# Optimization experiments

Hardware: AMD Instinct MI355X
Metric: run time of the kernel (lower is better)

The kernel has to match this reference:

```python
import jax, jax.numpy as jnp
import numpy as np

# quantization / activation scales (stand-ins for act_scales dict entries)
S_IN = 0.05      # in_proj:input
S_Z = 0.02       # in_proj:output (also gate/z scale)
S_U = 0.01       # x_proj:input (conv output scale)
S_DTLN = 0.02    # dt_layernorm:output
S_B = 0.02       # B_layernorm:output
S_C = 0.02       # C_layernorm:output
S_DT = 0.01      # dt_proj:output
S_Y = 0.01       # out_proj:input
EPS = 1e-6
R = 128          # time_step_rank
N = 16           # ssm_state_size


def qa(x, s):
    # simulate int8 activation quantization (values kept in fp32)
    return jnp.clip(jnp.round(x / s), -128.0, 127.0)


def qw(w):
    # per-tensor symmetric int8 weight quantization
    s = jnp.max(jnp.abs(w)) / 127.0
    return jnp.clip(jnp.round(w / s), -128.0, 127.0), s


def rmsnorm_q(x, w, s):
    x = x.astype(jnp.float32)
    x = x * jax.lax.rsqrt(jnp.mean(x * x, axis=-1, keepdims=True) + EPS)
    return qa(w * x, s)


def ssm_scan(u, dt, A, Bm, Cm):
    # u, dt: [B, D, S]; Bm, Cm: [B, S, N]; A: [D, N]
    def step(h, xs):
        dt_t, u_t, B_t, C_t = xs                     # [B,D],[B,D],[B,N],[B,N]
        dA = jnp.exp(dt_t[..., None] * A)            # [B,D,N]
        h = h * dA + (dt_t * u_t)[..., None] * B_t[:, None, :]
        y = jnp.einsum('bdn,bn->bd', h, C_t)
        return h, y
    Bsz, Dd, S = u.shape
    h0 = jnp.zeros((Bsz, Dd, A.shape[1]), u.dtype)
    xs = (jnp.moveaxis(dt, 2, 0), jnp.moveaxis(u, 2, 0),
          jnp.moveaxis(Bm, 1, 0), jnp.moveaxis(Cm, 1, 0))
    _, ys = jax.lax.scan(step, h0, xs)               # ys: [S,B,D]
    return jnp.moveaxis(ys, 0, 2)                    # [B,D,S]


def setup_inputs() -> dict:
    key = jax.random.key(0)
    ks = jax.random.split(key, 10)
    B, S, H, Din, K = 2, 2048, 2048, 4096, 4
    return {
        'hidden_states': jax.random.normal(ks[0], (B, S, H), jnp.float32),
        'in_proj_w': jax.random.normal(ks[1], (2 * Din, H), jnp.float32) * 0.02,
        'conv_w': jax.random.normal(ks[2], (Din, K), jnp.float32) * 0.1,
        'conv_b': jax.random.normal(ks[3], (Din,), jnp.float32) * 0.01,
        'x_proj_w': jax.random.normal(ks[4], (R + 2 * N, Din), jnp.float32) * 0.02,
        'dt_ln_w': jnp.ones((R,), jnp.float32),
        'B_ln_w': jnp.ones((N,), jnp.float32),
        'C_ln_w': jnp.ones((N,), jnp.float32),
        'dt_proj_w': jax.random.normal(ks[5], (Din, R), jnp.float32) * 0.05,
        'dt_bias': jax.random.normal(ks[6], (Din,), jnp.float32) * 0.5 - 4.0,
        'A_log': jnp.log(jnp.broadcast_to(jnp.arange(1, N + 1, dtype=jnp.float32), (Din, N))),
        'D_skip': jnp.ones((Din,), jnp.float32),
        'out_proj_w': jax.random.normal(ks[7], (H, Din), jnp.float32) * 0.02,
    }


def reference(hidden_states, in_proj_w, conv_w, conv_b, x_proj_w, dt_ln_w,
              B_ln_w, C_ln_w, dt_proj_w, dt_bias, A_log, D_skip, out_proj_w):
    # --- in_proj (W8A8B8O8), then seqlen-last layout [B, 2D, S] ---
    x_q = qa(hidden_states, S_IN)
    wq, ws = qw(in_proj_w)
    proj_q = qa((x_q @ wq.T) * (S_IN * ws), S_Z)          # [B,S,2D] int8-valued
    proj_q = jnp.swapaxes(proj_q, 1, 2)                   # [B,2D,S]
    Din = proj_q.shape[1] // 2
    hs_q, gate_q = proj_q[:, :Din], proj_q[:, Din:]

    # --- quantized causal depthwise conv1d + silu (QCausalConv1D) ---
    cwq, cws = qw(conv_w)
    K = conv_w.shape[1]
    conv_out = jax.lax.conv_general_dilated(
        hs_q, cwq[:, None, :], (1,), [(K - 1, 0)],
        dimension_numbers=('NCH', 'OIH', 'NCH'), feature_group_count=Din)
    conv_out = conv_out * (S_Z * cws) + conv_b[None, :, None]
    u_q = qa(jax.nn.silu(conv_out), S_U)                  # [B,Din,S]

    # --- x_proj (W8A8BF16OF16) -> dt/B/C, inner RMSNorms + quant ---
    xwq, xws = qw(x_proj_w)
    ssm_p = (jnp.swapaxes(u_q, 1, 2) @ xwq.T) * (S_U * xws)   # [B,S,R+2N] float
    dt_q = rmsnorm_q(ssm_p[..., :R], dt_ln_w, S_DTLN)
    B_q = rmsnorm_q(ssm_p[..., R:R + N], B_ln_w, S_B)
    C_q = rmsnorm_q(ssm_p[..., R + N:], C_ln_w, S_C)

    # --- dt_proj (W8A8B8O8, bias folded into scan) ---
    dwq, dws = qw(dt_proj_w)
    dt8 = qa((dt_q @ dwq.T) * (S_DTLN * dws), S_DT)       # [B,S,Din]
    dt = jax.nn.softplus(jnp.swapaxes(dt8, 1, 2) * S_DT + dt_bias[None, :, None])

    # --- selective scan (QSScan): dequantize, recur, gate ---
    u = u_q * S_U
    A = -jnp.exp(A_log)
    ys = ssm_scan(u, dt, A, B_q * S_B, C_q * S_C)         # [B,Din,S]
    ys = ys + u * D_skip[None, :, None]
    ys = ys * jax.nn.silu(gate_q * S_Z)

    # --- QAct + out_proj (W8A8BF16OF16) ---
    y_q = qa(jnp.swapaxes(ys, 1, 2), S_Y)                 # [B,S,Din]
    owq, ows = qw(out_proj_w)
    return (y_q @ owq.T) * (S_Y * ows)                    # [B,S,H]
```

## Files before the change

### kernel.cpp

```cpp
#include <hip/hip_runtime.h>
#include <stdint.h>

typedef signed char i8;
typedef int v4i __attribute__((ext_vector_type(4)));

#define S_IN  0.05f
#define S_Z   0.02f
#define S_U   0.01f
#define S_DTLN 0.02f
#define S_B   0.02f
#define S_C   0.02f
#define S_DT  0.01f
#define S_Y   0.01f

__device__ __forceinline__ int dot4(int a, int b, int c) {
    return __builtin_amdgcn_sdot4(a, b, c, false);
}

__device__ __forceinline__ float q8f(float x, float s) {
    float r = rintf(x / s);
    return fmaxf(-128.0f, fminf(127.0f, r));
}
__device__ __forceinline__ int q8i(float x, float s) { return (int)q8f(x, s); }

__device__ __forceinline__ float softplus_f(float x) {
    return __fadd_rn(fmaxf(x, 0.0f), log1pf(expf(-fabsf(x))));
}

__device__ __forceinline__ int sbyte_of(int w, int j) {
    return (int)(signed char)((unsigned)w >> (j * 8));
}

__device__ __forceinline__ void gload16(const i8* g, i8* lds) {
    __builtin_amdgcn_global_load_lds(
        (const __attribute__((address_space(1))) unsigned int*)g,
        (__attribute__((address_space(3))) unsigned int*)lds,
        16, 0, 0);
}

__global__ __launch_bounds__(256)
void k_maxabs(const float* __restrict__ w, long long n, unsigned* __restrict__ out) {
    unsigned m = 0;
    long long stride = (long long)gridDim.x * 256;
    for (long long i = (long long)blockIdx.x * 256 + threadIdx.x; i < n; i += stride)
        m = max(m, __float_as_uint(fabsf(w[i])));
    #pragma unroll
    for (int off = 32; off; off >>= 1) {
        unsigned o = (unsigned)__shfl_xor((int)m, off);
        m = max(m, o);
    }
    __shared__ unsigned sm[4];
    if ((threadIdx.x & 63) == 0) sm[threadIdx.x >> 6] = m;
    __syncthreads();
    if (threadIdx.x == 0) {
        unsigned r = max(max(sm[0], sm[1]), max(sm[2], sm[3]));
        atomicMax(out, r);
    }
}

__global__ __launch_bounds__(256)
void k_quant_w(const float* __restrict__ w, long long n,
               const unsigned* __restrict__ maxbits, i8* __restrict__ o) {
    long long i = ((long long)blockIdx.x * 256 + threadIdx.x) * 4;
    if (i >= n) return;
    float s = __uint_as_float(*maxbits) / 127.0f;
    float4 v = *(const float4*)(w + i);
    unsigned pk = ((unsigned)(q8i(v.x, s) & 255))
                | ((unsigned)(q8i(v.y, s) & 255) << 8)
                | ((unsigned)(q8i(v.z, s) & 255) << 16)
                | ((unsigned)(q8i(v.w, s) & 255) << 24);
    *(unsigned*)(o + i) = pk;
}

__global__ __launch_bounds__(256)
void k_quant_x(const float* __restrict__ x, long long n, float s, i8* __restrict__ o) {
    long long i = ((long long)blockIdx.x * 256 + threadIdx.x) * 4;
    if (i >= n) return;
    float4 v = *(const float4*)(x + i);
    unsigned pk = ((unsigned)(q8i(v.x, s) & 255))
                | ((unsigned)(q8i(v.y, s) & 255) << 8)
                | ((unsigned)(q8i(v.z, s) & 255) << 16)
                | ((unsigned)(q8i(v.w, s) & 255) << 24);
    *(unsigned*)(o + i) = pk;
}

template<int EPI>
__global__ __launch_bounds__(256)
void k_gemm(const i8* __restrict__ A, const i8* __restrict__ Bw,
            int M, int N, int K,
            const unsigned* __restrict__ wmaxbits,
            void* __restrict__ out0, void* __restrict__ out1) {
    __shared__ int As[64][17];
    __shared__ int Bs[64][17];
    const int tid = threadIdx.x;
    const int m0 = blockIdx.y << 6;
    const int n0 = blockIdx.x << 6;
    const int tx = tid & 15;
    const int ty = tid >> 4;
    const int ldr = tid >> 2;
    const int ldw = (tid & 3) << 2;
    int acc[4][4] = {};
    for (int k0 = 0; k0 < K; k0 += 64) {
        int4 av = *(const int4*)(A + (size_t)(m0 + ldr) * K + k0 + (ldw << 2));
        int4 bv = make_int4(0, 0, 0, 0);
        if (n0 + ldr < N)
            bv = *(const int4*)(Bw + (size_t)(n0 + ldr) * K + k0 + (ldw << 2));
        As[ldr][ldw + 0] = av.x; As[ldr][ldw + 1] = av.y;
        As[ldr][ldw + 2] = av.z; As[ldr][ldw + 3] = av.w;
        Bs[ldr][ldw + 0] = bv.x; Bs[ldr][ldw + 1] = bv.y;
        Bs[ldr][ldw + 2] = bv.z; Bs[ldr][ldw + 3] = bv.w;
        __syncthreads();
        #pragma unroll
        for (int kk = 0; kk < 16; kk++) {
            const int a0 = As[(ty << 2) + 0][kk];
            const int a1 = As[(ty << 2) + 1][kk];
            const int a2 = As[(ty << 2) + 2][kk];
            const int a3 = As[(ty << 2) + 3][kk];
            const int b0 = Bs[(tx << 2) + 0][kk];
            const int b1 = Bs[(tx << 2) + 1][kk];
            const int b2 = Bs[(tx << 2) + 2][kk];
            const int b3 = Bs[(tx << 2) + 3][kk];
            acc[0][0] = dot4(a0, b0, acc[0][0]); acc[0][1] = dot4(a0, b1, acc[0][1]);
            acc[0][2] = dot4(a0, b2, acc[0][2]); acc[0][3] = dot4(a0, b3, acc[0][3]);
            acc[1][0] = dot4(a1, b0, acc[1][0]); acc[1][1] = dot4(a1, b1, acc[1][1]);
            acc[1][2] = dot4(a1, b2, acc[1][2]); acc[1][3] = dot4(a1, b3, acc[1][3]);
            acc[2][0] = dot4(a2, b0, acc[2][0]); acc[2][1] = dot4(a2, b1, acc[2][1]);
            acc[2][2] = dot4(a2, b2, acc[2][2]); acc[2][3] = dot4(a2, b3, acc[2][3]);
            acc[3][0] = dot4(a3, b0, acc[3][0]); acc[3][1] = dot4(a3, b1, acc[3][1]);
            acc[3][2] = dot4(a3, b2, acc[3][2]); acc[3][3] = dot4(a3, b3, acc[3][3]);
        }
        __syncthreads();
    }
    const float wsc = __uint_as_float(*wmaxbits) / 127.0f;
    if constexpr (EPI == 1) {
        const float sc = S_U * wsc;
        float* O = (float*)out0;
        const int j0 = n0 + (tx << 2);
        #pragma unroll
        for (int r = 0; r < 4; r++) {
            const int m = m0 + (ty << 2) + r;
            if (j0 + 3 < N) {
                float4 v;
                v.x = (float)acc[r][0] * sc; v.y = (float)acc[r][1] * sc;
                v.z = (float)acc[r][2] * sc; v.w = (float)acc[r][3] * sc;
                *(float4*)(O + (size_t)m * N + j0) = v;
            } else {
                for (int c = 0; c < 4; c++)
                    if (j0 + c < N) O[(size_t)m * N + j0 + c] = (float)acc[r][c] * sc;
            }
        }
    }
}

template<int EPI>
__global__ __launch_bounds__(256)
void k_mgemm(const i8* __restrict__ A, const i8* __restrict__ Bw,
             int M, int N, int K,
             const unsigned* __restrict__ wmaxbits,
             void* __restrict__ out0, void* __restrict__ out1) {
    __shared__ i8 sA[8192];
    __shared__ i8 sB[8192];
    const int tid = threadIdx.x;
    const int w = tid >> 6;
    const int l = tid & 63;
    const int m0 = blockIdx.y << 7;
    const int n0 = blockIdx.x << 7;
    const int lr = l & 15;
    const int lk = l >> 4;
    const i8* gA0 = A  + (size_t)(m0 + (w * 16) + lr) * K + lk * 16;
    const i8* gA1 = A  + (size_t)(m0 + ((4 + w) * 16) + lr) * K + lk * 16;
    const i8* gB0 = Bw + (size_t)(n0 + (w * 16) + lr) * K + lk * 16;
    const i8* gB1 = Bw + (size_t)(n0 + ((4 + w) * 16) + lr) * K + lk * 16;
    i8* lA0 = sA + (w * 1024);
    i8* lA1 = sA + ((4 + w) * 1024);
    i8* lB0 = sB + (w * 1024);
    i8* lB1 = sB + ((4 + w) * 1024);
    const int mw = (w >> 1) * 4;
    const int nw = (w & 1) * 4;
    const int rdoff = lk * 256 + lr * 16;
    v4i acc[4][4] = {};
    for (int k0 = 0; k0 < K; k0 += 64) {
        gload16(gA0 + k0, lA0);
        gload16(gA1 + k0, lA1);
        gload16(gB0 + k0, lB0);
        gload16(gB1 + k0, lB1);
        __syncthreads();
        v4i af[4], bf[4];
        #pragma unroll
        for (int t = 0; t < 4; t++) {
            af[t] = *(const v4i*)(sA + (mw + t) * 1024 + rdoff);
            bf[t] = *(const v4i*)(sB + (nw + t) * 1024 + rdoff);
        }
        #pragma unroll
        for (int mt = 0; mt < 4; mt++)
            #pragma unroll
            for (int nt = 0; nt < 4; nt++)
                acc[mt][nt] = __builtin_amdgcn_mfma_i32_16x16x64_i8(af[mt], bf[nt], acc[mt][nt], 0, 0, 0);
        __syncthreads();
    }
    const float wsc = __uint_as_float(*wmaxbits) / 127.0f;
    const int m0w = m0 + (w >> 1) * 64;
    const int n0w = n0 + (w & 1) * 64;
    if constexpr (EPI == 0 || EPI == 2) {
        const float sc = (EPI == 0 ? S_IN : S_DTLN) * wsc;
        const float qs = (EPI == 0 ? S_Z : S_DT);
        const int b = m0w >> 11;
        #pragma unroll
        for (int nt = 0; nt < 4; nt++) {
            const int j = n0w + nt * 16 + lr;
            i8* dst;
            if constexpr (EPI == 0) dst = (j < 4096) ? (i8*)out0 : (i8*)out1;
            else dst = (i8*)out0;
            const int jj = j & 4095;
            #pragma unroll
            for (int mt = 0; mt < 4; mt++) {
                const int sbase = (m0w & 2047) + mt * 16 + lk * 4;
                unsigned pk = 0;
                #pragma unroll
                for (int r = 0; r < 4; r++) {
                    float v = (float)acc[mt][nt][r] * sc;
                    pk |= ((unsigned)(q8i(v, qs) & 255)) << (8 * r);
                }
                *(unsigned*)(dst + ((size_t)b * 4096 + jj) * 2048 + sbase) = pk;
            }
        }
    } else {
        const float sc = S_Y * wsc;
        float* O = (float*)out0;
        #pragma unroll
        for (int mt = 0; mt < 4; mt++)
            #pragma unroll
            for (int r = 0; r < 4; r++) {
                const int m = m0w + mt * 16 + lk * 4 + r;
                #pragma unroll
                for (int nt = 0; nt < 4; nt++)
                    O[(size_t)m * N + n0w + nt * 16 + lr] = (float)acc[mt][nt][r] * sc;
            }
    }
}

__global__ __launch_bounds__(256)
void k_conv(const i8* __restrict__ hsq, const i8* __restrict__ cwq,
            const float* __restrict__ conv_b, const unsigned* __restrict__ cmaxbits,
            i8* __restrict__ uq, i8* __restrict__ uqT) {
    __shared__ char lt[64][68];
    const int tid = threadIdx.x;
    const int b = blockIdx.z;
    const int d0 = blockIdx.y << 6;
    const int s0 = blockIdx.x << 6;
    const int dl = tid >> 2;
    const int sg = tid & 3;
    const int d = d0 + dl;
    const int sbase = s0 + (sg << 4);
    const i8* xp = hsq + ((size_t)b * 4096 + d) * 2048;
    int v[19];
    #pragma unroll
    for (int i = 0; i < 19; i++) {
        int s = sbase - 3 + i;
        v[i] = (s >= 0) ? (int)xp[s] : 0;
    }
    const unsigned cw = *(const unsigned*)(cwq + (size_t)d * 4);
    const int w0 = (int)(char)(cw & 255);
    const int w1 = (int)(char)((cw >> 8) & 255);
    const int w2 = (int)(char)((cw >> 16) & 255);
    const int w3 = (int)(char)((cw >> 24) & 255);
    const float cws = __uint_as_float(*cmaxbits) / 127.0f;
    const float sc = S_Z * cws;
    const float bias = conv_b[d];
    unsigned pk[4] = {0, 0, 0, 0};
    #pragma unroll
    for (int t = 0; t < 16; t++) {
        int acc = v[t] * w0 + v[t + 1] * w1 + v[t + 2] * w2 + v[t + 3] * w3;
        float f = __fadd_rn(__fmul_rn((float)acc, sc), bias);
        float sig = 1.0f / (1.0f + expf(-f));
        float sl = __fmul_rn(f, sig);
        int q = q8i(sl, S_U);
        pk[t >> 2] |= ((unsigned)(q & 255)) << ((t & 3) * 8);
        lt[(sg << 4) + t][dl] = (char)q;
    }
    *(int4*)(uq + ((size_t)b * 4096 + d) * 2048 + sbase) = make_int4(pk[0], pk[1], pk[2], pk[3]);
    __syncthreads();
    const int rr = tid >> 2;
    const int wg = tid & 3;
    const int* rp = (const int*)(&lt[rr][wg << 4]);
    int4 o; o.x = rp[0]; o.y = rp[1]; o.z = rp[2]; o.w = rp[3];
    *(int4*)(uqT + ((size_t)b * 2048 + s0 + rr) * 4096 + d0 + (wg << 4)) = o;
}

__global__ __launch_bounds__(64)
void k_rms(const float* __restrict__ p,
           const float* __restrict__ wdt, const float* __restrict__ wB, const float* __restrict__ wC,
           i8* __restrict__ dtq, i8* __restrict__ bqT, i8* __restrict__ cqT) {
    const int row = blockIdx.x;
    const int lane = threadIdx.x;
    const float* x = p + (size_t)row * 160;
    float a0 = x[lane], a1 = x[64 + lane];
    float bb = (lane < 16) ? x[128 + lane] : 0.0f;
    float cc = (lane < 16) ? x[144 + lane] : 0.0f;
    float sdt = __fadd_rn(__fmul_rn(a0, a0), __fmul_rn(a1, a1));
    float sB = __fmul_rn(bb, bb);
    float sC = __fmul_rn(cc, cc);
    #pragma unroll
    for (int off = 32; off; off >>= 1) {
        sdt = __fadd_rn(sdt, __shfl_xor(sdt, off));
        sB  = __fadd_rn(sB,  __shfl_xor(sB, off));
        sC  = __fadd_rn(sC,  __shfl_xor(sC, off));
    }
    float rdt = 1.0f / sqrtf(sdt / 128.0f + 1e-6f);
    float rB  = 1.0f / sqrtf(sB / 16.0f + 1e-6f);
    float rC  = 1.0f / sqrtf(sC / 16.0f + 1e-6f);
    dtq[(size_t)row * 128 + lane]      = (i8)q8i(__fmul_rn(wdt[lane],      __fmul_rn(a0, rdt)), S_DTLN);
    dtq[(size_t)row * 128 + 64 + lane] = (i8)q8i(__fmul_rn(wdt[64 + lane], __fmul_rn(a1, rdt)), S_DTLN);
    if (lane < 16) {
        size_t tpos = ((size_t)(row >> 11) * 16 + lane) * 2048 + (row & 2047);
        bqT[tpos] = (i8)q8i(__fmul_rn(wB[lane], __fmul_rn(bb, rB)), S_B);
        cqT[tpos] = (i8)q8i(__fmul_rn(wC[lane], __fmul_rn(cc, rC)), S_C);
    }
}

__global__ __launch_bounds__(256)
void k_lut_dt(const float* __restrict__ dt_bias, float* __restrict__ lut) {
    const int d = blockIdx.x;
    const int q = threadIdx.x;
    const float bias = dt_bias[d];
    lut[(size_t)d * 256 + q] =
        softplus_f(__fadd_rn(__fmul_rn((float)(q - 128), S_DT), bias));
}
__global__ __launch_bounds__(256)
void k_lut_silu(float* __restrict__ lut) {
    const int q = threadIdx.x;
    float gv = __fmul_rn((float)(q - 128), S_Z);
    float sg = __fmul_rn(gv, 1.0f / (1.0f + expf(-gv)));
    lut[q] = sg;
}

__global__ __launch_bounds__(256)
void k_scan3(const i8* __restrict__ dt8, const i8* __restrict__ uq, const i8* __restrict__ gq,
             const i8* __restrict__ BqT, const i8* __restrict__ CqT,
             const float* __restrict__ lut_dt, const float* __restrict__ lut_silu,
             const float* __restrict__ A_log, const float* __restrict__ D_skip,
             i8* __restrict__ yq) {
    const int g = blockIdx.x * 256 + threadIdx.x;
    const int n = g & 15;
    const int bd = g >> 4;
    const int d = bd & 4095;
    const int b = bd >> 12;
    const float Acoef = -expf(A_log[(size_t)d * 16 + n]);
    const float Dd = D_skip[d];
    const float* ldt = lut_dt + (size_t)d * 256;
    const v4i* dtp = (const v4i*)(dt8 + (size_t)bd * 2048);
    const v4i* up  = (const v4i*)(uq  + (size_t)bd * 2048);
    const v4i* gp  = (const v4i*)(gq  + (size_t)bd * 2048);
    const v4i* Bp  = (const v4i*)(BqT + ((size_t)b * 16 + n) * 2048);
    const v4i* Cp  = (const v4i*)(CqT + ((size_t)b * 16 + n) * 2048);
    i8* yp = yq + (size_t)b * 2048 * 4096 + d;
    float h = 0.0f;
    v4i dtw = dtp[0], uw = up[0], gw = gp[0], bw = Bp[0], cw = Cp[0];
    for (int t = 0; t < 128; t++) {
        v4i ndt, nu, ng, nb, nc;
        if (t < 127) { ndt = dtp[t + 1]; nu = up[t + 1]; ng = gp[t + 1]; nb = Bp[t + 1]; nc = Cp[t + 1]; }
        float dtv[16], dA[16];
        #pragma unroll
        for (int j = 0; j < 16; j++)
            dtv[j] = ldt[sbyte_of(dtw[j >> 2], j & 3) + 128];
        #pragma unroll
        for (int j = 0; j < 16; j++)
            dA[j] = expf(__fmul_rn(dtv[j], Acoef));
        float ysave = 0.0f;
        #pragma unroll
        for (int j = 0; j < 16; j++) {
            float uv = __fmul_rn((float)sbyte_of(uw[j >> 2], j & 3), S_U);
            float Bv = __fmul_rn((float)sbyte_of(bw[j >> 2], j & 3), S_B);
            float Cv = __fmul_rn((float)sbyte_of(cw[j >> 2], j & 3), S_C);
            h = __fadd_rn(__fmul_rn(h, dA[j]), __fmul_rn(__fmul_rn(dtv[j], uv), Bv));
            float y = __fmul_rn(h, Cv);
            y = __fadd_rn(y, __shfl_xor(y, 1));
            y = __fadd_rn(y, __shfl_xor(y, 2));
            y = __fadd_rn(y, __shfl_xor(y, 4));
            y = __fadd_rn(y, __shfl_xor(y, 8));
            if (j == n) ysave = y;
        }
        int uws = (n & 8) ? ((n & 4) ? uw[3] : uw[2]) : ((n & 4) ? uw[1] : uw[0]);
        int gws = (n & 8) ? ((n & 4) ? gw[3] : gw[2]) : ((n & 4) ? gw[1] : gw[0]);
        float uvn = __fmul_rn((float)(int)(signed char)((unsigned)uws >> ((n & 3) * 8)), S_U);
        int gb = (int)(signed char)((unsigned)gws >> ((n & 3) * 8));
        float ys = __fadd_rn(ysave, __fmul_rn(uvn, Dd));
        float sg = lut_silu[gb + 128];
        float vv = __fmul_rn(ys, sg);
        yp[(size_t)(t * 16 + n) * 4096] = (i8)q8i(vv, S_Y);
        if (t < 127) { dtw = ndt; uw = nu; gw = ng; bw = nb; cw = nc; }
    }
}

extern "C" void kernel_launch(void* const* d_in, const int* in_sizes, int n_in,
                              void* d_out, int out_size, void* d_ws, size_t ws_size,
                              hipStream_t stream) {
    const float* hidden   = (const float*)d_in[0];
    const float* in_proj  = (const float*)d_in[1];
    const float* conv_w   = (const float*)d_in[2];
    const float* conv_b   = (const float*)d_in[3];
    const float* x_proj   = (const float*)d_in[4];
    const float* dt_ln    = (const float*)d_in[5];
    const float* B_ln     = (const float*)d_in[6];
    const float* C_ln     = (const float*)d_in[7];
    const float* dt_proj  = (const float*)d_in[8];
    const float* dt_bias  = (const float*)d_in[9];
    const float* A_log    = (const float*)d_in[10];
    const float* D_skip   = (const float*)d_in[11];
    const float* out_proj = (const float*)d_in[12];
    float* out = (float*)d_out;

    char* ws = (char*)d_ws;
    unsigned* scales = (unsigned*)ws;
    i8* WQ   = (i8*)(ws + 256);
    i8* XQ   = (i8*)(ws + 16777472);
    i8* HSQ  = (i8*)(ws + 25166080);
    char* S0 = ws + 41943296;
    float* SSMP = (float*)S0;
    i8* DTQb = (i8*)(S0 + 2621440);
    i8* XWQ  = (i8*)(S0 + 3145728);
    i8* DWQ  = (i8*)(S0 + 3801088);
    i8* CWQ  = (i8*)(S0 + 4325376);
    float* LUTDT = (float*)S0;
    float* LUTSI = (float*)(S0 + 4194304);
    i8* BQT  = (i8*)(S0 + 4341760);
    i8* CQT  = (i8*)(S0 + 4407296);

    i8* GQ = (i8*)d_out;
    i8* UQ = (i8*)d_out + 16777216;
    i8* UQT = WQ;
    i8* OWQ = XQ;
    i8* DT8 = HSQ;
    i8* YQ  = WQ;

    hipMemsetAsync(scales, 0, 256, stream);

    k_maxabs<<<2048, 256, 0, stream>>>(in_proj, 16777216LL, scales + 0);
    k_maxabs<<<64,   256, 0, stream>>>(conv_w,  16384LL,    scales + 1);
    k_maxabs<<<512,  256, 0, stream>>>(x_proj,  655360LL,   scales + 2);
    k_maxabs<<<512,  256, 0, stream>>>(dt_proj, 524288LL,   scales + 3);
    k_maxabs<<<1024, 256, 0, stream>>>(out_proj, 8388608LL, scales + 4);

    k_quant_w<<<16384, 256, 0, stream>>>(in_proj, 16777216LL, scales + 0, WQ);
    k_quant_w<<<16,    256, 0, stream>>>(conv_w,  16384LL,    scales + 1, CWQ);
    k_quant_w<<<640,   256, 0, stream>>>(x_proj,  655360LL,   scales + 2, XWQ);
    k_quant_w<<<512,   256, 0, stream>>>(dt_proj, 524288LL,   scales + 3, DWQ);
    k_quant_x<<<8192,  256, 0, stream>>>(hidden,  8388608LL,  S_IN, XQ);

    k_mgemm<0><<<dim3(64, 32), 256, 0, stream>>>(XQ, WQ, 4096, 8192, 2048, scales + 0, HSQ, GQ);

    k_quant_w<<<8192, 256, 0, stream>>>(out_proj, 8388608LL, scales + 4, OWQ);

    dim3 gc(32, 64, 2);
    k_conv<<<gc, 256, 0, stream>>>(HSQ, CWQ, conv_b, scales + 1, UQ, UQT);

    dim3 g2(3, 64);
    k_gemm<1><<<g2, 256, 0, stream>>>(UQT, XWQ, 4096, 160, 4096, scales + 2, SSMP, nullptr);

    k_rms<<<4096, 64, 0, stream>>>(SSMP, dt_ln, B_ln, C_ln, DTQb, BQT, CQT);

    k_mgemm<2><<<dim3(32, 32), 256, 0, stream>>>(DTQb, DWQ, 4096, 4096, 128, scales + 3, DT8, nullptr);

    k_lut_dt<<<4096, 256, 0, stream>>>(dt_bias, LUTDT);
    k_lut_silu<<<1, 256, 0, stream>>>(LUTSI);

    k_scan3<<<512, 256, 0, stream>>>(DT8, UQ, GQ, BQT, CQT, LUTDT, LUTSI, A_log, D_skip, YQ);

    k_mgemm<3><<<dim3(16, 32), 256, 0, stream>>>(YQ, OWQ, 4096, 2048, 4096, scales + 4, out, nullptr);
}
```

Baseline: 787.8 us.

## Route x_proj through matrix-core GEMM and batch scan output reductions

The x_proj GEMM moves from the scalar sdot4 tiled kernel to the MFMA-based k_mgemm path. The weight is zero-padded to 256 rows in a fresh buffer, and a new epilogue writes only the first 160 columns. Separately, the scan kernel's 16 per-step shuffle-reduction chains (4 shuffles each) become a recursive-halving butterfly that exchanges half the partial sums at each level, so each lane ends with its own state's sum using fewer shuffles. The cost is an extra memset, wasted compute on the padded columns, and more register pressure in the scan.

```diff
diff --git a/kernel.cpp b/kernel.cpp
--- a/kernel.cpp
+++ b/kernel.cpp
@@ -12,10 +12,6 @@
 #define S_C   0.02f
 #define S_DT  0.01f
 #define S_Y   0.01f
-
-__device__ __forceinline__ int dot4(int a, int b, int c) {
-    return __builtin_amdgcn_sdot4(a, b, c, false);
-}
 
 __device__ __forceinline__ float q8f(float x, float s) {
     float r = rintf(x / s);
@@ -82,74 +78,6 @@
                 | ((unsigned)(q8i(v.z, s) & 255) << 16)
                 | ((unsigned)(q8i(v.w, s) & 255) << 24);
     *(unsigned*)(o + i) = pk;
-}
-
-template<int EPI>
-__global__ __launch_bounds__(256)
-void k_gemm(const i8* __restrict__ A, const i8* __restrict__ Bw,
-            int M, int N, int K,
-            const unsigned* __restrict__ wmaxbits,
-            void* __restrict__ out0, void* __restrict__ out1) {
-    __shared__ int As[64][17];
-    __shared__ int Bs[64][17];
-    const int tid = threadIdx.x;
-    const int m0 = blockIdx.y << 6;
-    const int n0 = blockIdx.x << 6;
-    const int tx = tid & 15;
-    const int ty = tid >> 4;
-    const int ldr = tid >> 2;
-    const int ldw = (tid & 3) << 2;
-    int acc[4][4] = {};
-    for (int k0 = 0; k0 < K; k0 += 64) {
-        int4 av = *(const int4*)(A + (size_t)(m0 + ldr) * K + k0 + (ldw << 2));
-        int4 bv = make_int4(0, 0, 0, 0);
-        if (n0 + ldr < N)
-            bv = *(const int4*)(Bw + (size_t)(n0 + ldr) * K + k0 + (ldw << 2));
-        As[ldr][ldw + 0] = av.x; As[ldr][ldw + 1] = av.y;
-        As[ldr][ldw + 2] = av.z; As[ldr][ldw + 3] = av.w;
-        Bs[ldr][ldw + 0] = bv.x; Bs[ldr][ldw + 1] = bv.y;
-        Bs[ldr][ldw + 2] = bv.z; Bs[ldr][ldw + 3] = bv.w;
-        __syncthreads();
-        #pragma unroll
-        for (int kk = 0; kk < 16; kk++) {
-            const int a0 = As[(ty << 2) + 0][kk];
-            const int a1 = As[(ty << 2) + 1][kk];
-            const int a2 = As[(ty << 2) + 2][kk];
-            const int a3 = As[(ty << 2) + 3][kk];
-            const int b0 = Bs[(tx << 2) + 0][kk];
-            const int b1 = Bs[(tx << 2) + 1][kk];
-            const int b2 = Bs[(tx << 2) + 2][kk];
-            const int b3 = Bs[(tx << 2) + 3][kk];
-            acc[0][0] = dot4(a0, b0, acc[0][0]); acc[0][1] = dot4(a0, b1, acc[0][1]);
-            acc[0][2] = dot4(a0, b2, acc[0][2]); acc[0][3] = dot4(a0, b3, acc[0][3]);
-            acc[1][0] = dot4(a1, b0, acc[1][0]); acc[1][1] = dot4(a1, b1, acc[1][1]);
-            acc[1][2] = dot4(a1, b2, acc[1][2]); acc[1][3] = dot4(a1, b3, acc[1][3]);
-            acc[2][0] = dot4(a2, b0, acc[2][0]); acc[2][1] = dot4(a2, b1, acc[2][1]);
-            acc[2][2] = dot4(a2, b2, acc[2][2]); acc[2][3] = dot4(a2, b3, acc[2][3]);
-            acc[3][0] = dot4(a3, b0, acc[3][0]); acc[3][1] = dot4(a3, b1, acc[3][1]);
-            acc[3][2] = dot4(a3, b2, acc[3][2]); acc[3][3] = dot4(a3, b3, acc[3][3]);
-        }
-        __syncthreads();
-    }
-    const float wsc = __uint_as_float(*wmaxbits) / 127.0f;
-    if constexpr (EPI == 1) {
-        const float sc = S_U * wsc;
-        float* O = (float*)out0;
-        const int j0 = n0 + (tx << 2);
-        #pragma unroll
-        for (int r = 0; r < 4; r++) {
-            const int m = m0 + (ty << 2) + r;
-            if (j0 + 3 < N) {
-                float4 v;
-                v.x = (float)acc[r][0] * sc; v.y = (float)acc[r][1] * sc;
-                v.z = (float)acc[r][2] * sc; v.w = (float)acc[r][3] * sc;
-                *(float4*)(O + (size_t)m * N + j0) = v;
-            } else {
-                for (int c = 0; c < 4; c++)
-                    if (j0 + c < N) O[(size_t)m * N + j0 + c] = (float)acc[r][c] * sc;
-            }
-        }
-    }
 }
 
 template<int EPI>
@@ -224,6 +152,21 @@
                 *(unsigned*)(dst + ((size_t)b * 4096 + jj) * 2048 + sbase) = pk;
             }
         }
+    } else if constexpr (EPI == 1) {
+        const float sc = S_U * wsc;
+        float* O = (float*)out0;
+        #pragma unroll
+        for (int mt = 0; mt < 4; mt++)
+            #pragma unroll
+            for (int r = 0; r < 4; r++) {
+                const int m = m0w + mt * 16 + lk * 4 + r;
+                #pragma unroll
+                for (int nt = 0; nt < 4; nt++) {
+                    const int j = n0w + nt * 16 + lr;
+                    if (j < 160)
+                        O[(size_t)m * 160 + j] = (float)acc[mt][nt][r] * sc;
+                }
+            }
     } else {
         const float sc = S_Y * wsc;
         float* O = (float*)out0;
@@ -335,7 +278,7 @@
 }
 
 __global__ __launch_bounds__(256)
-void k_scan3(const i8* __restrict__ dt8, const i8* __restrict__ uq, const i8* __restrict__ gq,
+void k_scan4(const i8* __restrict__ dt8, const i8* __restrict__ uq, const i8* __restrict__ gq,
              const i8* __restrict__ BqT, const i8* __restrict__ CqT,
              const float* __restrict__ lut_dt, const float* __restrict__ lut_silu,
              const float* __restrict__ A_log, const float* __restrict__ D_skip,
@@ -359,26 +302,59 @@
     for (int t = 0; t < 128; t++) {
         v4i ndt, nu, ng, nb, nc;
         if (t < 127) { ndt = dtp[t + 1]; nu = up[t + 1]; ng = gp[t + 1]; nb = Bp[t + 1]; nc = Cp[t + 1]; }
-        float dtv[16], dA[16];
+        float dtv[16], dA[16], pj[16], Cv[16], y[16];
         #pragma unroll
         for (int j = 0; j < 16; j++)
             dtv[j] = ldt[sbyte_of(dtw[j >> 2], j & 3) + 128];
         #pragma unroll
         for (int j = 0; j < 16; j++)
             dA[j] = expf(__fmul_rn(dtv[j], Acoef));
-        float ysave = 0.0f;
         #pragma unroll
         for (int j = 0; j < 16; j++) {
             float uv = __fmul_rn((float)sbyte_of(uw[j >> 2], j & 3), S_U);
             float Bv = __fmul_rn((float)sbyte_of(bw[j >> 2], j & 3), S_B);
-            float Cv = __fmul_rn((float)sbyte_of(cw[j >> 2], j & 3), S_C);
-            h = __fadd_rn(__fmul_rn(h, dA[j]), __fmul_rn(__fmul_rn(dtv[j], uv), Bv));
-            float y = __fmul_rn(h, Cv);
-            y = __fadd_rn(y, __shfl_xor(y, 1));
-            y = __fadd_rn(y, __shfl_xor(y, 2));
-            y = __fadd_rn(y, __shfl_xor(y, 4));
-            y = __fadd_rn(y, __shfl_xor(y, 8));
-            if (j == n) ysave = y;
+            Cv[j] = __fmul_rn((float)sbyte_of(cw[j >> 2], j & 3), S_C);
+            pj[j] = __fmul_rn(__fmul_rn(dtv[j], uv), Bv);
+        }
+        #pragma unroll
+        for (int j = 0; j < 16; j++) {
+            h = __fadd_rn(__fmul_rn(h, dA[j]), pj[j]);
+            y[j] = __fmul_rn(h, Cv[j]);
+        }
+        float w8[8];
+        #pragma unroll
+        for (int i = 0; i < 8; i++) {
+            float a = y[2 * i], bq = y[2 * i + 1];
+            float snd = (n & 1) ? a : bq;
+            float rcv = __shfl_xor(snd, 1);
+            float kept = (n & 1) ? bq : a;
+            w8[i] = __fadd_rn(kept, rcv);
+        }
+        float w4[4];
+        #pragma unroll
+        for (int i = 0; i < 4; i++) {
+            float a = w8[2 * i], bq = w8[2 * i + 1];
+            float snd = (n & 2) ? a : bq;
+            float rcv = __shfl_xor(snd, 2);
+            float kept = (n & 2) ? bq : a;
+            w4[i] = __fadd_rn(kept, rcv);
+        }
+        float w2[2];
+        #pragma unroll
+        for (int i = 0; i < 2; i++) {
+            float a = w4[2 * i], bq = w4[2 * i + 1];
+            float snd = (n & 4) ? a : bq;
+            float rcv = __shfl_xor(snd, 4);
+            float kept = (n & 4) ? bq : a;
+            w2[i] = __fadd_rn(kept, rcv);
+        }
+        float ysave;
+        {
+            float a = w2[0], bq = w2[1];
+            float snd = (n & 8) ? a : bq;
+            float rcv = __shfl_xor(snd, 8);
+            float kept = (n & 8) ? bq : a;
+            ysave = __fadd_rn(kept, rcv);
         }
         int uws = (n & 8) ? ((n & 4) ? uw[3] : uw[2]) : ((n & 4) ? uw[1] : uw[0]);
         int gws = (n & 8) ? ((n & 4) ? gw[3] : gw[2]) : ((n & 4) ? gw[1] : gw[0]);
@@ -417,14 +393,14 @@
     i8* HSQ  = (i8*)(ws + 25166080);
     char* S0 = ws + 41943296;
     float* SSMP = (float*)S0;
-    i8* DTQb = (i8*)(S0 + 2621440);
-    i8* XWQ  = (i8*)(S0 + 3145728);
-    i8* DWQ  = (i8*)(S0 + 3801088);
-    i8* CWQ  = (i8*)(S0 + 4325376);
+    i8* XWQp = (i8*)(S0 + 2621440);
+    i8* DTQb = (i8*)(S0 + 3670016);
+    i8* DWQ  = (i8*)(S0 + 4194304);
+    i8* CWQ  = (i8*)(S0 + 4718592);
+    float* LUTSI = (float*)(S0 + 4734976);
+    i8* BQT  = (i8*)(S0 + 4736000);
+    i8* CQT  = (i8*)(S0 + 4801536);
     float* LUTDT = (float*)S0;
-    float* LUTSI = (float*)(S0 + 4194304);
-    i8* BQT  = (i8*)(S0 + 4341760);
-    i8* CQT  = (i8*)(S0 + 4407296);
 
     i8* GQ = (i8*)d_out;
     i8* UQ = (i8*)d_out + 16777216;
@@ -434,6 +410,7 @@
     i8* YQ  = WQ;
 
     hipMemsetAsync(scales, 0, 256, stream);
+    hipMemsetAsync(XWQp, 0, 1048576, stream);
 
     k_maxabs<<<2048, 256, 0, stream>>>(in_proj, 16777216LL, scales + 0);
     k_maxabs<<<64,   256, 0, stream>>>(conv_w,  16384LL,    scales + 1);
@@ -443,7 +420,7 @@
 
     k_quant_w<<<16384, 256, 0, stream>>>(in_proj, 16777216LL, scales + 0, WQ);
     k_quant_w<<<16,    256, 0, stream>>>(conv_w,  16384LL,    scales + 1, CWQ);
-    k_quant_w<<<640,   256, 0, stream>>>(x_proj,  655360LL,   scales + 2, XWQ);
+    k_quant_w<<<640,   256, 0, stream>>>(x_proj,  655360LL,   scales + 2, XWQp);
     k_quant_w<<<512,   256, 0, stream>>>(dt_proj, 524288LL,   scales + 3, DWQ);
     k_quant_x<<<8192,  256, 0, stream>>>(hidden,  8388608LL,  S_IN, XQ);
 
@@ -454,8 +431,7 @@
     dim3 gc(32, 64, 2);
     k_conv<<<gc, 256, 0, stream>>>(HSQ, CWQ, conv_b, scales + 1, UQ, UQT);
 
-    dim3 g2(3, 64);
-    k_gemm<1><<<g2, 256, 0, stream>>>(UQT, XWQ, 4096, 160, 4096, scales + 2, SSMP, nullptr);
+    k_mgemm<1><<<dim3(2, 32), 256, 0, stream>>>(UQT, XWQp, 4096, 256, 4096, scales + 2, SSMP, nullptr);
 
     k_rms<<<4096, 64, 0, stream>>>(SSMP, dt_ln, B_ln, C_ln, DTQb, BQT, CQT);
 
@@ -464,7 +440,7 @@
     k_lut_dt<<<4096, 256, 0, stream>>>(dt_bias, LUTDT);
     k_lut_silu<<<1, 256, 0, stream>>>(LUTSI);
 
-    k_scan3<<<512, 256, 0, stream>>>(DT8, UQ, GQ, BQT, CQT, LUTDT, LUTSI, A_log, D_skip, YQ);
+    k_scan4<<<512, 256, 0, stream>>>(DT8, UQ, GQ, BQT, CQT, LUTDT, LUTSI, A_log, D_skip, YQ);
 
     k_mgemm<3><<<dim3(16, 32), 256, 0, stream>>>(YQ, OWQ, 4096, 2048, 4096, scales + 4, out, nullptr);
 }
```

After: 717.9 us. -8.9%, faster.
